# Kernel optimization log

Hardware: AMD Instinct MI355X
Metric: run time of the kernel (lower is better)

## Reference

```python
import jax, jax.numpy as jnp
import numpy as np

B, C, H, L, D = 128, 5, 50, 32, 300
VOCAB = 50000
KN = 20  # len(torch.arange(-0.9, 1.1, 0.1))
EPS = 1e-8


def setup_inputs() -> dict:
    key = jax.random.key(0)
    k1, k2, k3, k4 = jax.random.split(key, 4)
    return {
        "candidate_title": jax.random.randint(k1, (B, C, L), 0, VOCAB),
        "clicked_title": jax.random.randint(k2, (B, H, L), 0, VOCAB),
        "embedding": jax.random.normal(k3, (VOCAB, D), dtype=jnp.float32),
        "ltr_w": jax.random.normal(k4, (1, H * KN), dtype=jnp.float32) * 0.03,
        "ltr_b": jnp.zeros((1,), dtype=jnp.float32),
    }


def reference(candidate_title, clicked_title, embedding, ltr_w, ltr_b):
    mus = jnp.arange(KN, dtype=jnp.float32) * 0.1 - 0.9
    sigmas = jnp.concatenate([jnp.full((KN - 1,), 0.1, dtype=jnp.float32),
                              jnp.array([0.001], dtype=jnp.float32)])

    ce = embedding[candidate_title]            # [B,C,L,D]
    he = embedding[clicked_title]              # [B,H,L,D]
    # torch CosineSimilarity: dot / (clamp(||a||,eps)*clamp(||b||,eps))
    cn = ce / jnp.clip(jnp.linalg.norm(ce, axis=-1, keepdims=True), EPS)
    hn = he / jnp.clip(jnp.linalg.norm(he, axis=-1, keepdims=True), EPS)
    sim = jnp.einsum('bcid,bhjd->bchij', cn, hn)  # [B,C,H,L,L] fusion matrix

    # kernel pooling: sum over columns j per Gaussian kernel, then log-sum over rows i
    pooled = jnp.stack(
        [jnp.sum(jnp.exp(-(sim - mus[k]) ** 2 / (2.0 * sigmas[k] ** 2)), axis=-1)
         for k in range(KN)], axis=-1)          # [B,C,H,L,KN]
    pv = jnp.sum(jnp.log(jnp.clip(pooled, 1e-10)), axis=-2)  # [B,C,H,KN]
    pv = pv.reshape(B, C, H * KN)

    score = pv @ ltr_w.T + ltr_b               # [B,C,1]
    return jax.nn.log_softmax(score, axis=1)[..., 0]  # [B,C]
```

## Files before the change

kernel.cpp:

```cpp
#include <hip/hip_runtime.h>
#include <hip/hip_bf16.h>

#define VOCABN 50000
#define BN 128
#define CN 5
#define HN 50
#define LN 32
#define DN 300
#define DP 320
#define KNN 20

typedef __bf16    bf16x8 __attribute__((ext_vector_type(8)));
typedef float     f32x4  __attribute__((ext_vector_type(4)));
typedef float     f32x2  __attribute__((ext_vector_type(2)));
typedef ushort    u16x8  __attribute__((ext_vector_type(8)));

#if __has_builtin(__builtin_amdgcn_exp2f)
#define FEXP2 __builtin_amdgcn_exp2f
#else
#define FEXP2 exp2f
#endif
#if __has_builtin(__builtin_amdgcn_logf)
#define FLOG2 __builtin_amdgcn_logf
#else
#define FLOG2 log2f
#endif

#define LOG2E 1.4426950408889634f
#define LN2F  0.6931471805599453f

__global__ __launch_bounds__(256) void knorm_embed2(const float* __restrict__ emb,
                                                    ushort* __restrict__ tabo) {
    const int t    = threadIdx.x;
    const int lane = t & 63;
    const int w    = t >> 6;
    const int v    = blockIdx.x * 4 + w;
    const float* row = emb + (size_t)v * DN;
    const float4* r4 = (const float4*)row;

    float4 x = r4[lane];
    float ss = x.x * x.x + x.y * x.y + x.z * x.z + x.w * x.w;
    if (lane < 11) {
        float4 y = r4[64 + lane];
        ss += y.x * y.x + y.y * y.y + y.z * y.z + y.w * y.w;
    }
    #pragma unroll
    for (int off = 32; off; off >>= 1) ss += __shfl_xor(ss, off);
    const float scale = 1.0f / fmaxf(sqrtf(ss), 1e-8f);

    if (lane < 40) {
        u16x8 u;
        #pragma unroll
        for (int j = 0; j < 8; ++j) {
            int e = lane * 8 + j;
            float f = (e < DN) ? row[e] * scale : 0.f;
            __hip_bfloat16 h = __float2bfloat16(f);
            u[j] = *(ushort*)&h;
        }
        *(u16x8*)(tabo + (size_t)v * DP + lane * 8) = u;
    }
}

__device__ __forceinline__ int paddr(int row, int c) {
    return ((row >> 1) << 7) + ((((c + ((row & 1) << 2))) ^ ((row >> 1) & 7)) << 4);
}
__device__ __forceinline__ bf16x8 ldP(const char* buf, int row, int c) {
    return *(const bf16x8*)(buf + paddr(row, c));
}

__global__ __launch_bounds__(320, 4) void knrm_fused12(const int* __restrict__ cand,
                                                       const int* __restrict__ clik,
                                                       const ushort* __restrict__ tab,
                                                       const float* __restrict__ ltr_w,
                                                       float* __restrict__ score) {
    __shared__ __align__(16) char smem[40960];

    const int t    = threadIdx.x;
    const int lane = t & 63;
    const int w    = t >> 6;
    const int bid  = (blockIdx.x & 7) * 800 + (blockIdx.x >> 3);
    const int b    = bid / HN;
    const int h    = bid % HN;

    char* arena = smem + w * 8192;
    char* Ab[2] = { arena,        arena + 2048 };
    char* Bb[2] = { arena + 4096, arena + 6144 };

    const int m15 = lane & 63 & 15;
    const int g4  = lane >> 4;

    const int r0 = lane >> 2, c0 = lane & 3;
    const int r1 = 16 + r0;
    const int tA0 = cand[b * (CN * LN) + w * LN + r0];
    const int tA1 = cand[b * (CN * LN) + w * LN + r1];
    const int tB0 = clik[b * (HN * LN) + h * LN + r0];
    const int tB1 = clik[b * (HN * LN) + h * LN + r1];
    const char* sA0 = (const char*)tab + (size_t)tA0 * (DP * 2) + c0 * 16;
    const char* sA1 = (const char*)tab + (size_t)tA1 * (DP * 2) + c0 * 16;
    const char* sB0 = (const char*)tab + (size_t)tB0 * (DP * 2) + c0 * 16;
    const char* sB1 = (const char*)tab + (size_t)tB1 * (DP * 2) + c0 * 16;
    const int dA0 = paddr(r0, c0), dA1 = paddr(r1, c0);
    const int dB0 = paddr(r0, c0), dB1 = paddr(r1, c0);

    f32x4 acc[2][2];
    #pragma unroll
    for (int at = 0; at < 2; ++at)
        #pragma unroll
        for (int jg = 0; jg < 2; ++jg)
            acc[at][jg] = (f32x4){0.f, 0.f, 0.f, 0.f};

    {
        int4 q0 = *(const int4*)sA0;
        int4 q1 = *(const int4*)sA1;
        int4 q2 = *(const int4*)sB0;
        int4 q3 = *(const int4*)sB1;
        *(int4*)(Ab[0] + dA0) = q0;
        *(int4*)(Ab[0] + dA1) = q1;
        *(int4*)(Bb[0] + dB0) = q2;
        *(int4*)(Bb[0] + dB1) = q3;
    }
    int4 p0 = *(const int4*)(sA0 + 64);
    int4 p1 = *(const int4*)(sA1 + 64);
    int4 p2 = *(const int4*)(sB0 + 64);
    int4 p3 = *(const int4*)(sB1 + 64);

    #pragma unroll
    for (int ss = 0; ss < 10; ++ss) {
        const char* A = Ab[ss & 1];
        const char* B = Bb[ss & 1];

        bf16x8 af0 = ldP(A, m15,      g4);
        bf16x8 af1 = ldP(A, 16 + m15, g4);
        bf16x8 bf0 = ldP(B, m15,      g4);
        bf16x8 bf1 = ldP(B, 16 + m15, g4);

        if (ss < 9) {
            char* An = Ab[(ss + 1) & 1];
            char* Bn = Bb[(ss + 1) & 1];
            *(int4*)(An + dA0) = p0;
            *(int4*)(An + dA1) = p1;
            *(int4*)(Bn + dB0) = p2;
            *(int4*)(Bn + dB1) = p3;
        }
        if (ss < 8) {
            const int so = (ss + 2) * 64;
            p0 = *(const int4*)(sA0 + so);
            p1 = *(const int4*)(sA1 + so);
            p2 = *(const int4*)(sB0 + so);
            p3 = *(const int4*)(sB1 + so);
        }

        acc[0][0] = __builtin_amdgcn_mfma_f32_16x16x32_bf16(af0, bf0, acc[0][0], 0, 0, 0);
        acc[0][1] = __builtin_amdgcn_mfma_f32_16x16x32_bf16(af0, bf1, acc[0][1], 0, 0, 0);
        acc[1][0] = __builtin_amdgcn_mfma_f32_16x16x32_bf16(af1, bf0, acc[1][0], 0, 0, 0);
        acc[1][1] = __builtin_amdgcn_mfma_f32_16x16x32_bf16(af1, bf1, acc[1][1], 0, 0, 0);
    }

    const float C1   = 10.0f * LOG2E;
    const float C2   = -50.0f * LOG2E;
    const float AK19 = 849.3218002880191f;
    static const float CkT[10] = {
        1.0f, 0.6065306597126334f, 0.1353352832366127f, 0.011108996538242306f,
        3.3546262790251185e-4f, 3.7266531720786709e-6f, 1.5229979744712628e-8f,
        2.2897348456191135e-11f, 1.2664165549094176e-14f, 2.576757109154981e-18f };

    float* sb = (float*)arena;

    #pragma unroll
    for (int at = 0; at < 2; ++at)
        #pragma unroll
        for (int jgl = 0; jgl < 2; ++jgl)
            #pragma unroll
            for (int r = 0; r < 4; ++r)
                sb[(at * 16 + g4 * 4 + r) * 33 + jgl * 16 + m15] = acc[at][jgl][r];

    const int hi = lane >> 5;
    const float* sp = sb + (lane & 31) * 33 + hi * 16;

    f32x2 Qp[9];
    #pragma unroll
    for (int j = 0; j < 9; ++j) Qp[j] = (f32x2){0.f, 0.f};
    float Q9 = 0.f, Q19 = 0.f;

    #pragma unroll
    for (int ec = 0; ec < 4; ++ec) {
        f32x4 v = *(const f32x4*)(sp + ec * 4);
        #pragma unroll
        for (int e = 0; e < 4; ++e) {
            float s  = v[e];
            float cs = C1 * s;
            float tt = FEXP2(cs);
            float uu = FEXP2(-cs);
            float e0 = FEXP2(C2 * (s * s));
            Q9 += e0;
            f32x2 tu = {tt, uu};
            f32x2 pm = {e0, e0};
            #pragma unroll
            for (int j = 0; j < 9; ++j) { pm *= tu; Qp[j] += pm; }
            float d = fmaf(s, AK19, -AK19);
            Q19 += FEXP2(-(d * d));
        }
    }

    #pragma unroll
    for (int j = 0; j < 9; ++j) {
        Qp[j].x += __shfl_xor(Qp[j].x, 32);
        Qp[j].y += __shfl_xor(Qp[j].y, 32);
    }
    Q9  += __shfl_xor(Q9, 32);
    Q19 += __shfl_xor(Q19, 32);

    const float* wrow = ltr_w + h * KNN;
    float q0 = hi ? Q19 : Q9;
    float w0 = wrow[hi ? 19 : 9];
    float res = w0 * FLOG2(fmaxf(q0, 1e-10f));
    #pragma unroll
    for (int j = 1; j <= 9; ++j) {
        float q  = hi ? Qp[j - 1].x : Qp[j - 1].y;
        float wk = wrow[hi ? (9 + j) : (9 - j)];
        res += wk * FLOG2(fmaxf(q * CkT[j], 1e-10f));
    }

    res *= LN2F;
    #pragma unroll
    for (int off = 32; off; off >>= 1) res += __shfl_xor(res, off);
    if (lane == 0) atomicAdd(&score[b * CN + w], res);
}

__global__ __launch_bounds__(128) void knrm_final(const float* __restrict__ score,
                                                  float* __restrict__ out) {
    int b = threadIdx.x;
    if (b < BN) {
        float s[CN];
        float m = -1e30f;
        #pragma unroll
        for (int c = 0; c < CN; ++c) { s[c] = score[b * CN + c]; m = fmaxf(m, s[c]); }
        float sum = 0.f;
        #pragma unroll
        for (int c = 0; c < CN; ++c) sum += FEXP2((s[c] - m) * LOG2E);
        float lse = m + FLOG2(sum) * LN2F;
        #pragma unroll
        for (int c = 0; c < CN; ++c) out[b * CN + c] = s[c] - lse;
    }
}

extern "C" void kernel_launch(void* const* d_in, const int* in_sizes, int n_in,
                              void* d_out, int out_size, void* d_ws, size_t ws_size,
                              hipStream_t stream) {
    const int*   cand  = (const int*)d_in[0];
    const int*   clik  = (const int*)d_in[1];
    const float* emb   = (const float*)d_in[2];
    const float* ltr_w = (const float*)d_in[3];
    float* out = (float*)d_out;

    const size_t TAB_B = (size_t)VOCABN * DP * 2;

    ushort* tab  = (ushort*)d_ws;
    float*  scre = (float*)((char*)d_ws + TAB_B);

    hipMemsetAsync(scre, 0, BN * CN * sizeof(float), stream);
    knorm_embed2<<<VOCABN / 4, 256, 0, stream>>>(emb, tab);
    knrm_fused12<<<BN * HN, 320, 0, stream>>>(cand, clik, tab, ltr_w, scre);
    knrm_final<<<1, 128, 0, stream>>>(scre, out);
}
```

Baseline: 130.8 us.

## Single-buffer LDS staging, raise occupancy, skip narrow-kernel exp, fold memset

Drops the per-wave LDS double buffer for a single buffer, which roughly halves shared memory per block. Launch bounds go from 4 to 8 blocks per CU to raise occupancy. Each wave now reads its fragments before overwriting the buffer in the same iteration, so correctness depends on LDS operations staying in program order within the wave. The sharp sigma=0.001 kernel term is only evaluated when some similarity in the wave exceeds 0.99; below that its contribution underflows and is lost under the 1e-10 clamp anyway. The score-zeroing memset is folded into the embedding-normalisation kernel, removing one launch.

```diff
diff --git a/kernel.cpp b/kernel.cpp
--- a/kernel.cpp
+++ b/kernel.cpp
@@ -30,8 +30,13 @@
 #define LN2F  0.6931471805599453f
 
 __global__ __launch_bounds__(256) void knorm_embed2(const float* __restrict__ emb,
-                                                    ushort* __restrict__ tabo) {
+                                                    ushort* __restrict__ tabo,
+                                                    float* __restrict__ scre) {
     const int t    = threadIdx.x;
+    if (blockIdx.x == 0) {
+        scre[t] = 0.f; scre[t + 256] = 0.f;
+        if (t < 128) scre[t + 512] = 0.f;
+    }
     const int lane = t & 63;
     const int w    = t >> 6;
     const int v    = blockIdx.x * 4 + w;
@@ -68,12 +73,12 @@
     return *(const bf16x8*)(buf + paddr(row, c));
 }
 
-__global__ __launch_bounds__(320, 4) void knrm_fused12(const int* __restrict__ cand,
+__global__ __launch_bounds__(320, 8) void knrm_fused13(const int* __restrict__ cand,
                                                        const int* __restrict__ clik,
                                                        const ushort* __restrict__ tab,
                                                        const float* __restrict__ ltr_w,
                                                        float* __restrict__ score) {
-    __shared__ __align__(16) char smem[40960];
+    __shared__ __align__(16) char smem[21760];
 
     const int t    = threadIdx.x;
     const int lane = t & 63;
@@ -82,11 +87,11 @@
     const int b    = bid / HN;
     const int h    = bid % HN;
 
-    char* arena = smem + w * 8192;
-    char* Ab[2] = { arena,        arena + 2048 };
-    char* Bb[2] = { arena + 4096, arena + 6144 };
-
-    const int m15 = lane & 63 & 15;
+    char* arena = smem + w * 4352;
+    char* Ab = arena;
+    char* Bb = arena + 2048;
+
+    const int m15 = lane & 15;
     const int g4  = lane >> 4;
 
     const int r0 = lane >> 2, c0 = lane & 3;
@@ -99,8 +104,7 @@
     const char* sA1 = (const char*)tab + (size_t)tA1 * (DP * 2) + c0 * 16;
     const char* sB0 = (const char*)tab + (size_t)tB0 * (DP * 2) + c0 * 16;
     const char* sB1 = (const char*)tab + (size_t)tB1 * (DP * 2) + c0 * 16;
-    const int dA0 = paddr(r0, c0), dA1 = paddr(r1, c0);
-    const int dB0 = paddr(r0, c0), dB1 = paddr(r1, c0);
+    const int d0 = paddr(r0, c0), d1 = paddr(r1, c0);
 
     f32x4 acc[2][2];
     #pragma unroll
@@ -114,10 +118,10 @@
         int4 q1 = *(const int4*)sA1;
         int4 q2 = *(const int4*)sB0;
         int4 q3 = *(const int4*)sB1;
-        *(int4*)(Ab[0] + dA0) = q0;
-        *(int4*)(Ab[0] + dA1) = q1;
-        *(int4*)(Bb[0] + dB0) = q2;
-        *(int4*)(Bb[0] + dB1) = q3;
+        *(int4*)(Ab + d0) = q0;
+        *(int4*)(Ab + d1) = q1;
+        *(int4*)(Bb + d0) = q2;
+        *(int4*)(Bb + d1) = q3;
     }
     int4 p0 = *(const int4*)(sA0 + 64);
     int4 p1 = *(const int4*)(sA1 + 64);
@@ -126,21 +130,16 @@
 
     #pragma unroll
     for (int ss = 0; ss < 10; ++ss) {
-        const char* A = Ab[ss & 1];
-        const char* B = Bb[ss & 1];
-
-        bf16x8 af0 = ldP(A, m15,      g4);
-        bf16x8 af1 = ldP(A, 16 + m15, g4);
-        bf16x8 bf0 = ldP(B, m15,      g4);
-        bf16x8 bf1 = ldP(B, 16 + m15, g4);
+        bf16x8 af0 = ldP(Ab, m15,      g4);
+        bf16x8 af1 = ldP(Ab, 16 + m15, g4);
+        bf16x8 bf0 = ldP(Bb, m15,      g4);
+        bf16x8 bf1 = ldP(Bb, 16 + m15, g4);
 
         if (ss < 9) {
-            char* An = Ab[(ss + 1) & 1];
-            char* Bn = Bb[(ss + 1) & 1];
-            *(int4*)(An + dA0) = p0;
-            *(int4*)(An + dA1) = p1;
-            *(int4*)(Bn + dB0) = p2;
-            *(int4*)(Bn + dB1) = p3;
+            *(int4*)(Ab + d0) = p0;
+            *(int4*)(Ab + d1) = p1;
+            *(int4*)(Bb + d0) = p2;
+            *(int4*)(Bb + d1) = p3;
         }
         if (ss < 8) {
             const int so = (ss + 2) * 64;
@@ -197,8 +196,14 @@
             f32x2 pm = {e0, e0};
             #pragma unroll
             for (int j = 0; j < 9; ++j) { pm *= tu; Qp[j] += pm; }
-            float d = fmaf(s, AK19, -AK19);
-            Q19 += FEXP2(-(d * d));
+        }
+        float m4 = fmaxf(fmaxf(v[0], v[1]), fmaxf(v[2], v[3]));
+        if (__any(m4 > 0.99f)) {
+            #pragma unroll
+            for (int e = 0; e < 4; ++e) {
+                float d = fmaf(v[e], AK19, -AK19);
+                Q19 += FEXP2(-(d * d));
+            }
         }
     }
 
@@ -258,8 +263,7 @@
     ushort* tab  = (ushort*)d_ws;
     float*  scre = (float*)((char*)d_ws + TAB_B);
 
-    hipMemsetAsync(scre, 0, BN * CN * sizeof(float), stream);
-    knorm_embed2<<<VOCABN / 4, 256, 0, stream>>>(emb, tab);
-    knrm_fused12<<<BN * HN, 320, 0, stream>>>(cand, clik, tab, ltr_w, scre);
+    knorm_embed2<<<VOCABN / 4, 256, 0, stream>>>(emb, tab, scre);
+    knrm_fused13<<<BN * HN, 320, 0, stream>>>(cand, clik, tab, ltr_w, scre);
     knrm_final<<<1, 128, 0, stream>>>(scre, out);
 }
```

Result: faster. 126.2 us (-3.5%).
